# Kernel optimization log

Hardware: AMD Instinct MI355X
Metric: run time of the kernel (lower is better)

Reference implementation:

```python
import jax, jax.numpy as jnp
import numpy as np

NUM_EXPERTS = 64
TOP_K = 2
CAP_FACTOR = 1.0


def setup_inputs() -> dict:
    key = jax.random.key(0)
    k1, k2 = jax.random.split(key)
    x = jax.random.normal(k1, (8192, 4096), dtype=jnp.float32)
    wg = jax.random.normal(k2, (NUM_EXPERTS, 4096), dtype=jnp.float32) * 0.02
    return {"x": x, "wg": wg}


def reference(x, wg):
    # x: [S, M] tokens, wg: [E, M] gate weight (Linear, no bias)
    S, M = x.shape
    E, K = NUM_EXPERTS, TOP_K
    capacity = K * int(CAP_FACTOR * ((S + E - 1) // E))  # static

    logits = jnp.einsum('sm,em->se', x, wg)            # [S, E]
    gates = jax.nn.softmax(logits, axis=1)             # [S, E]
    _, topk_idx = jax.lax.top_k(logits, K)             # [S, K]

    masks = jax.nn.one_hot(topk_idx, E, dtype=x.dtype)  # [S, K, E]
    gates_s = jnp.einsum('se,ske->sk', gates, masks)    # [S, K]

    # load-balancing loss (fp32 path of load_balance)
    me = jnp.sum(gates, axis=0)                         # [E]
    ce = jnp.sum(masks[:, 0], axis=0)                   # [E]
    l_loss = jnp.sum(me * ce) * (E / (S * S))

    # capacity locations: cumsum-sub-one per k, offset by counts of earlier k's
    locs = jnp.cumsum(masks, axis=0) - 1.0              # [S, K, E]
    counts = jnp.sum(masks, axis=0)                     # [K, E]
    acc = jnp.concatenate([jnp.zeros((1, E), x.dtype),
                           jnp.cumsum(counts, axis=0)[:-1]], axis=0)  # [K, E]
    locs = locs + acc[None, :, :]
    loc_s = jnp.einsum('ske,ske->sk', locs, masks).astype(jnp.int32)  # [S, K]

    # postnorm gate normalization (top_k > 1)
    eps = jnp.finfo(gates_s.dtype).eps
    gates_n = gates_s / jnp.clip(jnp.sum(gates_s, axis=1, keepdims=True), eps)

    idx = topk_idx.astype(jnp.int32)                    # [S, K]
    valid = (loc_s >= 0) & (loc_s < capacity)           # [S, K]
    pos = jnp.where(valid, idx * capacity + loc_s, 0)   # [S, K] flat slot ids

    # encode: scatter tokens (unweighted, is_postnorm=True) into [E*capacity, M]
    contrib = jnp.where(valid[..., None], x[:, None, :], 0.0)  # [S, K, M]
    dispatched = jnp.zeros((E * capacity, M), x.dtype)
    dispatched = dispatched.at[pos.reshape(-1)].add(contrib.reshape(-1, M))

    # expert_fn = identity (world_size=1, routing pipeline is the op under test)
    expert_output = dispatched                          # [E*capacity, M]

    # decode: gather back and combine with normalized gates
    gathered = expert_output[pos.reshape(-1)].reshape(S, K, M)
    out = jnp.einsum('sk,skm->sm', gates_n * valid.astype(x.dtype), gathered)
    return out, l_loss
```

## Files before the change

kernel.cpp:

```cpp
#include <hip/hip_runtime.h>
#include <math.h>

#define S_TOK 8192
#define M_DIM 4096
#define NEXP 64
#define CAPACITY 256
#define NCHUNK 128
#define KS 8
#define KSL 512
#define BT 64
#define BK 32
#define NC (KSL / BK)

__global__ __launch_bounds__(256) void k_logits(
    const float* __restrict__ x, const float* __restrict__ wg,
    float* __restrict__ part)
{
    __shared__ float xs[2][BK * 64];
    __shared__ float wsl[2][BK * 64];
    const int tid = threadIdx.x;
    const int tile = blockIdx.x >> 3;
    const int ks   = blockIdx.x & 7;
    const int t0 = tile * BT;
    const int kb = ks * KSL;

    const int tx = tid & 15;
    const int ty = tid >> 4;

    float4 rx[2], rw[2];
    auto ld = [&](int kc) {
        #pragma unroll
        for (int i = 0; i < 2; ++i) {
            const int item = tid + 256 * i;
            const int r = item >> 3, kq = item & 7;
            rx[i] = *(const float4*)(x  + (size_t)(t0 + r) * M_DIM + kc + 4 * kq);
            rw[i] = *(const float4*)(wg + (size_t)r       * M_DIM + kc + 4 * kq);
        }
    };
    auto st = [&](int buf) {
        #pragma unroll
        for (int i = 0; i < 2; ++i) {
            const int item = tid + 256 * i;
            const int r = item >> 3, kq = item & 7;
            const int quad = r >> 2, lo = r & 3;
            const float vx[4] = {rx[i].x, rx[i].y, rx[i].z, rx[i].w};
            const float vw[4] = {rw[i].x, rw[i].y, rw[i].z, rw[i].w};
            #pragma unroll
            for (int j = 0; j < 4; ++j) {
                const int row = 4 * kq + j;
                const int addr = row * 64 + ((quad ^ kq) << 2) + lo;
                xs[buf][addr]  = vx[j];
                wsl[buf][addr] = vw[j];
            }
        }
    };

    float acc[4][4] = {};
    ld(kb);
    st(0);
    __syncthreads();
    for (int c = 0; c < NC; ++c) {
        const int buf = c & 1;
        if (c + 1 < NC) ld(kb + (c + 1) * BK);
        #pragma unroll 8
        for (int kk = 0; kk < BK; ++kk) {
            const int sw = kk >> 2;
            const float4 a = *(const float4*)&xs [buf][kk * 64 + ((ty ^ sw) << 2)];
            const float4 b = *(const float4*)&wsl[buf][kk * 64 + ((tx ^ sw) << 2)];
            const float av[4] = {a.x, a.y, a.z, a.w};
            const float bv[4] = {b.x, b.y, b.z, b.w};
            #pragma unroll
            for (int i = 0; i < 4; ++i)
                #pragma unroll
                for (int j = 0; j < 4; ++j)
                    acc[i][j] = fmaf(av[i], bv[j], acc[i][j]);
        }
        __syncthreads();
        if (c + 1 < NC) st(buf ^ 1);
        __syncthreads();
    }

    #pragma unroll
    for (int i = 0; i < 4; ++i) {
        float4 v;
        v.x = acc[i][0]; v.y = acc[i][1]; v.z = acc[i][2]; v.w = acc[i][3];
        *(float4*)(part + ((size_t)ks * S_TOK + t0 + 4 * ty + i) * NEXP + 4 * tx) = v;
    }
}

__global__ __launch_bounds__(256) void k_reduce(
    const float* __restrict__ part, float* __restrict__ me_g,
    int* __restrict__ idx0_g, int* __restrict__ idx1_g,
    float* __restrict__ gn0_g, float* __restrict__ gn1_g)
{
    __shared__ float me_sh[NEXP];
    const int tid = threadIdx.x;
    if (tid < NEXP) me_sh[tid] = 0.f;
    __syncthreads();

    const int wv = tid >> 6, lane = tid & 63;
    float me_acc = 0.f;
    for (int i = 0; i < 8; ++i) {
        const int t = blockIdx.x * 32 + wv * 8 + i;
        float lg = 0.f;
        #pragma unroll
        for (int s = 0; s < KS; ++s)
            lg += part[((size_t)s * S_TOK + t) * NEXP + lane];

        float v = lg; int id = lane;
        #pragma unroll
        for (int off = 32; off > 0; off >>= 1) {
            float v2 = __shfl_xor(v, off);
            int   i2 = __shfl_xor(id, off);
            if (v2 > v || (v2 == v && i2 < id)) { v = v2; id = i2; }
        }
        const float mx = v; const int i0 = id;

        const float p = expf(lg - mx);
        float sum = p;
        #pragma unroll
        for (int off = 32; off > 0; off >>= 1) sum += __shfl_xor(sum, off);
        me_acc += p / sum;

        float v1 = (lane == i0) ? -INFINITY : lg; int id1 = lane;
        #pragma unroll
        for (int off = 32; off > 0; off >>= 1) {
            float v2 = __shfl_xor(v1, off);
            int   i2 = __shfl_xor(id1, off);
            if (v2 > v1 || (v2 == v1 && i2 < id1)) { v1 = v2; id1 = i2; }
        }

        const float g0 = 1.0f / sum;
        const float g1 = expf(v1 - mx) / sum;
        const float den = fmaxf(g0 + g1, 1.1920929e-07f);
        if (lane == 0) {
            idx0_g[t] = i0;
            idx1_g[t] = id1;
            gn0_g[t] = g0 / den;
            gn1_g[t] = g1 / den;
        }
    }
    atomicAdd(&me_sh[lane], me_acc);
    __syncthreads();
    if (tid < NEXP) atomicAdd(&me_g[tid], me_sh[tid]);
}

__global__ __launch_bounds__(64) void k_rank(
    const int* __restrict__ idx0_g, const int* __restrict__ idx1_g,
    int* __restrict__ rank0_g, int* __restrict__ rank1_g,
    int* __restrict__ cnt_g )
{
    const int lane = threadIdx.x;
    const int chunk = blockIdx.x;
    const int s = chunk * 64 + lane;
    const int e0 = idx0_g[s], e1 = idx1_g[s];
    const unsigned long long lt = (1ull << lane) - 1ull;

    int r0 = 0, r1 = 0, c0 = 0, c1 = 0;
    #pragma unroll
    for (int e = 0; e < 64; ++e) {
        unsigned long long m0 = __ballot(e0 == e);
        unsigned long long m1 = __ballot(e1 == e);
        if (e0 == e) r0 = __popcll(m0 & lt);
        if (e1 == e) r1 = __popcll(m1 & lt);
        if (lane == e) { c0 = __popcll(m0); c1 = __popcll(m1); }
    }
    rank0_g[s] = r0;
    rank1_g[s] = r1;
    cnt_g[chunk * 64 + lane] = c0;
    cnt_g[NCHUNK * 64 + chunk * 64 + lane] = c1;
}

__global__ __launch_bounds__(256) void k_scan(
    const int* __restrict__ cnt_g, int* __restrict__ base_g,
    int* __restrict__ tot0_g, const float* __restrict__ me_g,
    float* __restrict__ loss_out)
{
    const int wv = threadIdx.x >> 6, lane = threadIdx.x & 63;
    const int g = blockIdx.x * 4 + wv;
    const int k = g >> 6, e = g & 63;

    const int c0 = cnt_g[(k * NCHUNK + 2 * lane)     * 64 + e];
    const int c1 = cnt_g[(k * NCHUNK + 2 * lane + 1) * 64 + e];
    const int s = c0 + c1;
    int incl = s;
    #pragma unroll
    for (int d = 1; d < 64; d <<= 1) {
        int v = __shfl_up(incl, d);
        if (lane >= d) incl += v;
    }
    const int excl = incl - s;
    base_g[(k * NCHUNK + 2 * lane)     * 64 + e] = excl;
    base_g[(k * NCHUNK + 2 * lane + 1) * 64 + e] = excl + c0;
    const int total = __shfl(incl, 63);
    if (k == 0 && lane == 0) {
        tot0_g[e] = total;
        atomicAdd(loss_out, me_g[e] * (float)total * 9.5367431640625e-07f);
    }
}

__global__ __launch_bounds__(256) void k_weight(
    const int* __restrict__ idx0_g, const int* __restrict__ idx1_g,
    const float* __restrict__ gn0_g, const float* __restrict__ gn1_g,
    const int* __restrict__ rank0_g, const int* __restrict__ rank1_g,
    const int* __restrict__ base_g, const int* __restrict__ tot0_g,
    float* __restrict__ w_g)
{
    const int s = blockIdx.x * 256 + threadIdx.x;
    const int chunk = s >> 6;
    const int e0 = idx0_g[s], e1 = idx1_g[s];
    const int loc0 = base_g[chunk * 64 + e0] + rank0_g[s];
    const int loc1 = base_g[(NCHUNK + chunk) * 64 + e1] + rank1_g[s] + tot0_g[e1];
    float w = 0.f;
    if (loc0 < CAPACITY) w += gn0_g[s];
    if (loc1 < CAPACITY) w += gn1_g[s];
    w_g[s] = w;
}

__global__ __launch_bounds__(256) void k_out(
    const float* __restrict__ x, const float* __restrict__ w_g,
    float* __restrict__ out)
{
    const int s = blockIdx.x;
    const float w = w_g[s];
    const float4* xr = (const float4*)(x + (size_t)s * M_DIM);
    float4* o = (float4*)(out + (size_t)s * M_DIM);
    #pragma unroll
    for (int i = 0; i < 4; ++i) {
        float4 v = xr[threadIdx.x + 256 * i];
        v.x *= w; v.y *= w; v.z *= w; v.w *= w;
        o[threadIdx.x + 256 * i] = v;
    }
}

extern "C" void kernel_launch(void* const* d_in, const int* in_sizes, int n_in,
                              void* d_out, int out_size, void* d_ws, size_t ws_size,
                              hipStream_t stream)
{
    const float* x  = (const float*)d_in[0];
    const float* wg = (const float*)d_in[1];
    float* out = (float*)d_out;
    float* loss = out + (size_t)S_TOK * M_DIM;

    float* part = (float*)d_ws;
    float* me   = part + (size_t)KS * S_TOK * NEXP;
    int*  idx0  = (int*)(me + NEXP);
    int*  idx1  = idx0 + S_TOK;
    float* gn0  = (float*)(idx1 + S_TOK);
    float* gn1  = gn0 + S_TOK;
    int*  rank0 = (int*)(gn1 + S_TOK);
    int*  rank1 = rank0 + S_TOK;
    int*  cnt   = rank1 + S_TOK;
    int*  base  = cnt + 2 * NCHUNK * 64;
    int*  tot0  = base + 2 * NCHUNK * 64;
    float* wtok = (float*)(tot0 + NEXP);

    hipMemsetAsync(me, 0, NEXP * sizeof(float), stream);
    hipMemsetAsync(loss, 0, sizeof(float), stream);

    k_logits<<<128 * KS, 256, 0, stream>>>(x, wg, part);
    k_reduce<<<S_TOK / 32, 256, 0, stream>>>(part, me, idx0, idx1, gn0, gn1);
    k_rank<<<NCHUNK, 64, 0, stream>>>(idx0, idx1, rank0, rank1, cnt);
    k_scan<<<32, 256, 0, stream>>>(cnt, base, tot0, me, loss);
    k_weight<<<S_TOK / 256, 256, 0, stream>>>(idx0, idx1, gn0, gn1,
                                              rank0, rank1, base, tot0, wtok);
    k_out<<<S_TOK, 256, 0, stream>>>(x, wtok, out);
}
```

Before: 310.8 us.

## Restructure logits GEMM to stream gate weights, fuse routing and scan kernels

The logits kernel now stages only x in LDS (XOR-swizzled per token), and each wave reads 16 expert rows of wg directly from global/cache as float4s, so each thread computes one token against 16 experts. The reduce and rank kernels are merged into a per-chunk routing kernel that packs indices and ranks into one int. The scan, loss and weight kernels are merged into a single 1024-thread block. This cuts launch count and intermediate global traffic. The risks are a serialized single-block finish stage and heavier global loads of wg inside the GEMM inner loop.

```diff
diff --git a/kernel.cpp b/kernel.cpp
--- a/kernel.cpp
+++ b/kernel.cpp
@@ -8,100 +8,105 @@
 #define NCHUNK 128
 #define KS 8
 #define KSL 512
-#define BT 64
-#define BK 32
-#define NC (KSL / BK)
+#define BKL 32
+#define NCL (KSL / BKL)
 
 __global__ __launch_bounds__(256) void k_logits(
     const float* __restrict__ x, const float* __restrict__ wg,
     float* __restrict__ part)
 {
-    __shared__ float xs[2][BK * 64];
-    __shared__ float wsl[2][BK * 64];
+    __shared__ float xt[2][BKL * 64];
     const int tid = threadIdx.x;
     const int tile = blockIdx.x >> 3;
-    const int ks   = blockIdx.x & 7;
-    const int t0 = tile * BT;
+    const int ks = blockIdx.x & 7;
+    const int t0 = tile * 64;
     const int kb = ks * KSL;
-
-    const int tx = tid & 15;
-    const int ty = tid >> 4;
-
-    float4 rx[2], rw[2];
+    const int wave = __builtin_amdgcn_readfirstlane(tid >> 6);
+    const int lane = tid & 63;
+    const int e0 = wave * 16;
+
+    float4 rx[2];
     auto ld = [&](int kc) {
         #pragma unroll
         for (int i = 0; i < 2; ++i) {
             const int item = tid + 256 * i;
-            const int r = item >> 3, kq = item & 7;
-            rx[i] = *(const float4*)(x  + (size_t)(t0 + r) * M_DIM + kc + 4 * kq);
-            rw[i] = *(const float4*)(wg + (size_t)r       * M_DIM + kc + 4 * kq);
+            const int tok = item >> 3, kq = item & 7;
+            rx[i] = *(const float4*)(x + (size_t)(t0 + tok) * M_DIM + kc + 4 * kq);
         }
     };
     auto st = [&](int buf) {
         #pragma unroll
         for (int i = 0; i < 2; ++i) {
             const int item = tid + 256 * i;
-            const int r = item >> 3, kq = item & 7;
-            const int quad = r >> 2, lo = r & 3;
-            const float vx[4] = {rx[i].x, rx[i].y, rx[i].z, rx[i].w};
-            const float vw[4] = {rw[i].x, rw[i].y, rw[i].z, rw[i].w};
+            const int tok = item >> 3, kq = item & 7;
+            const float v[4] = {rx[i].x, rx[i].y, rx[i].z, rx[i].w};
             #pragma unroll
             for (int j = 0; j < 4; ++j) {
-                const int row = 4 * kq + j;
-                const int addr = row * 64 + ((quad ^ kq) << 2) + lo;
-                xs[buf][addr]  = vx[j];
-                wsl[buf][addr] = vw[j];
+                const int k = 4 * kq + j;
+                xt[buf][k * 64 + (tok ^ k)] = v[j];
             }
         }
     };
 
-    float acc[4][4] = {};
+    float acc[16] = {};
     ld(kb);
     st(0);
     __syncthreads();
-    for (int c = 0; c < NC; ++c) {
+    for (int c = 0; c < NCL; ++c) {
         const int buf = c & 1;
-        if (c + 1 < NC) ld(kb + (c + 1) * BK);
-        #pragma unroll 8
-        for (int kk = 0; kk < BK; ++kk) {
-            const int sw = kk >> 2;
-            const float4 a = *(const float4*)&xs [buf][kk * 64 + ((ty ^ sw) << 2)];
-            const float4 b = *(const float4*)&wsl[buf][kk * 64 + ((tx ^ sw) << 2)];
-            const float av[4] = {a.x, a.y, a.z, a.w};
-            const float bv[4] = {b.x, b.y, b.z, b.w};
-            #pragma unroll
-            for (int i = 0; i < 4; ++i)
-                #pragma unroll
-                for (int j = 0; j < 4; ++j)
-                    acc[i][j] = fmaf(av[i], bv[j], acc[i][j]);
+        if (c + 1 < NCL) ld(kb + (c + 1) * BKL);
+        const float* wrow = wg + (size_t)e0 * M_DIM + kb + c * BKL;
+        #pragma unroll
+        for (int k4 = 0; k4 < BKL; k4 += 4) {
+            float4 wv[16];
+            #pragma unroll
+            for (int e = 0; e < 16; ++e)
+                wv[e] = *(const float4*)(wrow + (size_t)e * M_DIM + k4);
+            float a[4];
+            #pragma unroll
+            for (int j = 0; j < 4; ++j) {
+                const int k = k4 + j;
+                a[j] = xt[buf][k * 64 + (lane ^ k)];
+            }
+            #pragma unroll
+            for (int e = 0; e < 16; ++e) {
+                acc[e] = fmaf(a[0], wv[e].x, acc[e]);
+                acc[e] = fmaf(a[1], wv[e].y, acc[e]);
+                acc[e] = fmaf(a[2], wv[e].z, acc[e]);
+                acc[e] = fmaf(a[3], wv[e].w, acc[e]);
+            }
         }
         __syncthreads();
-        if (c + 1 < NC) st(buf ^ 1);
+        if (c + 1 < NCL) st(buf ^ 1);
         __syncthreads();
     }
-
-    #pragma unroll
-    for (int i = 0; i < 4; ++i) {
+    float* po = part + ((size_t)ks * S_TOK + t0 + lane) * NEXP + e0;
+    #pragma unroll
+    for (int j = 0; j < 4; ++j) {
         float4 v;
-        v.x = acc[i][0]; v.y = acc[i][1]; v.z = acc[i][2]; v.w = acc[i][3];
-        *(float4*)(part + ((size_t)ks * S_TOK + t0 + 4 * ty + i) * NEXP + 4 * tx) = v;
-    }
-}
-
-__global__ __launch_bounds__(256) void k_reduce(
+        v.x = acc[4*j]; v.y = acc[4*j+1]; v.z = acc[4*j+2]; v.w = acc[4*j+3];
+        *(float4*)(po + 4 * j) = v;
+    }
+}
+
+__global__ __launch_bounds__(256) void k_route(
     const float* __restrict__ part, float* __restrict__ me_g,
-    int* __restrict__ idx0_g, int* __restrict__ idx1_g,
-    float* __restrict__ gn0_g, float* __restrict__ gn1_g)
+    int* __restrict__ pack_g, float* __restrict__ g0_g, float* __restrict__ g1_g,
+    int* __restrict__ cnt_g )
 {
     __shared__ float me_sh[NEXP];
+    __shared__ int   idxs[64];
+    __shared__ float g0s[64], g1s[64];
     const int tid = threadIdx.x;
+    const int wv = tid >> 6, lane = tid & 63;
+    const int chunk = blockIdx.x;
     if (tid < NEXP) me_sh[tid] = 0.f;
     __syncthreads();
 
-    const int wv = tid >> 6, lane = tid & 63;
     float me_acc = 0.f;
-    for (int i = 0; i < 8; ++i) {
-        const int t = blockIdx.x * 32 + wv * 8 + i;
+    for (int i = 0; i < 16; ++i) {
+        const int tl = wv * 16 + i;
+        const int t = chunk * 64 + tl;
         float lg = 0.f;
         #pragma unroll
         for (int s = 0; s < KS; ++s)
@@ -134,87 +139,96 @@
         const float g1 = expf(v1 - mx) / sum;
         const float den = fmaxf(g0 + g1, 1.1920929e-07f);
         if (lane == 0) {
-            idx0_g[t] = i0;
-            idx1_g[t] = id1;
-            gn0_g[t] = g0 / den;
-            gn1_g[t] = g1 / den;
+            idxs[tl] = i0 | (id1 << 8);
+            g0s[tl] = g0 / den;
+            g1s[tl] = g1 / den;
         }
     }
     atomicAdd(&me_sh[lane], me_acc);
     __syncthreads();
     if (tid < NEXP) atomicAdd(&me_g[tid], me_sh[tid]);
-}
-
-__global__ __launch_bounds__(64) void k_rank(
-    const int* __restrict__ idx0_g, const int* __restrict__ idx1_g,
-    int* __restrict__ rank0_g, int* __restrict__ rank1_g,
-    int* __restrict__ cnt_g )
-{
-    const int lane = threadIdx.x;
-    const int chunk = blockIdx.x;
-    const int s = chunk * 64 + lane;
-    const int e0 = idx0_g[s], e1 = idx1_g[s];
-    const unsigned long long lt = (1ull << lane) - 1ull;
-
-    int r0 = 0, r1 = 0, c0 = 0, c1 = 0;
-    #pragma unroll
-    for (int e = 0; e < 64; ++e) {
-        unsigned long long m0 = __ballot(e0 == e);
-        unsigned long long m1 = __ballot(e1 == e);
-        if (e0 == e) r0 = __popcll(m0 & lt);
-        if (e1 == e) r1 = __popcll(m1 & lt);
-        if (lane == e) { c0 = __popcll(m0); c1 = __popcll(m1); }
-    }
-    rank0_g[s] = r0;
-    rank1_g[s] = r1;
-    cnt_g[chunk * 64 + lane] = c0;
-    cnt_g[NCHUNK * 64 + chunk * 64 + lane] = c1;
-}
-
-__global__ __launch_bounds__(256) void k_scan(
-    const int* __restrict__ cnt_g, int* __restrict__ base_g,
-    int* __restrict__ tot0_g, const float* __restrict__ me_g,
-    float* __restrict__ loss_out)
-{
-    const int wv = threadIdx.x >> 6, lane = threadIdx.x & 63;
-    const int g = blockIdx.x * 4 + wv;
-    const int k = g >> 6, e = g & 63;
-
-    const int c0 = cnt_g[(k * NCHUNK + 2 * lane)     * 64 + e];
-    const int c1 = cnt_g[(k * NCHUNK + 2 * lane + 1) * 64 + e];
-    const int s = c0 + c1;
-    int incl = s;
-    #pragma unroll
-    for (int d = 1; d < 64; d <<= 1) {
-        int v = __shfl_up(incl, d);
-        if (lane >= d) incl += v;
-    }
-    const int excl = incl - s;
-    base_g[(k * NCHUNK + 2 * lane)     * 64 + e] = excl;
-    base_g[(k * NCHUNK + 2 * lane + 1) * 64 + e] = excl + c0;
-    const int total = __shfl(incl, 63);
-    if (k == 0 && lane == 0) {
-        tot0_g[e] = total;
-        atomicAdd(loss_out, me_g[e] * (float)total * 9.5367431640625e-07f);
-    }
-}
-
-__global__ __launch_bounds__(256) void k_weight(
-    const int* __restrict__ idx0_g, const int* __restrict__ idx1_g,
-    const float* __restrict__ gn0_g, const float* __restrict__ gn1_g,
-    const int* __restrict__ rank0_g, const int* __restrict__ rank1_g,
-    const int* __restrict__ base_g, const int* __restrict__ tot0_g,
-    float* __restrict__ w_g)
-{
-    const int s = blockIdx.x * 256 + threadIdx.x;
-    const int chunk = s >> 6;
-    const int e0 = idx0_g[s], e1 = idx1_g[s];
-    const int loc0 = base_g[chunk * 64 + e0] + rank0_g[s];
-    const int loc1 = base_g[(NCHUNK + chunk) * 64 + e1] + rank1_g[s] + tot0_g[e1];
-    float w = 0.f;
-    if (loc0 < CAPACITY) w += gn0_g[s];
-    if (loc1 < CAPACITY) w += gn1_g[s];
-    w_g[s] = w;
+
+    if (wv == 0) {
+        const int pk = idxs[lane];
+        const int e0 = pk & 255, e1 = pk >> 8;
+        const unsigned long long lt = (1ull << lane) - 1ull;
+        int r0 = 0, r1 = 0, c0 = 0, c1 = 0;
+        #pragma unroll
+        for (int e = 0; e < 64; ++e) {
+            unsigned long long m0 = __ballot(e0 == e);
+            unsigned long long m1 = __ballot(e1 == e);
+            if (e0 == e) r0 = __popcll(m0 & lt);
+            if (e1 == e) r1 = __popcll(m1 & lt);
+            if (lane == e) { c0 = __popcll(m0); c1 = __popcll(m1); }
+        }
+        const int s = chunk * 64 + lane;
+        pack_g[s] = e0 | (e1 << 8) | (r0 << 16) | (r1 << 24);
+        g0_g[s] = g0s[lane];
+        g1_g[s] = g1s[lane];
+        cnt_g[chunk * 64 + lane] = c0;
+        cnt_g[(NCHUNK + chunk) * 64 + lane] = c1;
+    }
+}
+
+__global__ __launch_bounds__(1024) void k_finish(
+    const int* __restrict__ cnt_g, const int* __restrict__ pack_g,
+    const float* __restrict__ g0_g, const float* __restrict__ g1_g,
+    const float* __restrict__ me_g, float* __restrict__ wtok,
+    float* __restrict__ loss)
+{
+    __shared__ unsigned short base16[2][NCHUNK][NEXP];
+    __shared__ int ssum[8][128];
+    __shared__ int tot0s[NEXP];
+    __shared__ float lred[NEXP];
+    const int tid = threadIdx.x;
+    const int pair = tid & 127, seg = tid >> 7;
+    const int k = pair >> 6, e = pair & 63;
+
+    int cv[16], s = 0;
+    #pragma unroll
+    for (int c = 0; c < 16; ++c) {
+        cv[c] = cnt_g[(k * NCHUNK + seg * 16 + c) * 64 + e];
+        s += cv[c];
+    }
+    ssum[seg][pair] = s;
+    __syncthreads();
+
+    int segbase = 0, total = 0;
+    #pragma unroll
+    for (int s2 = 0; s2 < 8; ++s2) {
+        const int v = ssum[s2][pair];
+        if (s2 < seg) segbase += v;
+        total += v;
+    }
+    if (k == 0 && seg == 0) tot0s[e] = total;
+    int run = segbase;
+    #pragma unroll
+    for (int c = 0; c < 16; ++c) {
+        base16[k][seg * 16 + c][e] = (unsigned short)run;
+        run += cv[c];
+    }
+    __syncthreads();
+
+    if (tid < NEXP) lred[tid] = me_g[tid] * (float)tot0s[tid];
+    __syncthreads();
+    if (tid == 0) {
+        float t = 0.f;
+        for (int i = 0; i < NEXP; ++i) t += lred[i];
+        *loss = t * 9.5367431640625e-07f;
+    }
+
+    #pragma unroll
+    for (int j = 0; j < 8; ++j) {
+        const int t = j * 1024 + tid;
+        const int pk = pack_g[t];
+        const int e0 = pk & 63, e1 = (pk >> 8) & 63;
+        const int r0 = (pk >> 16) & 255, r1 = (pk >> 24) & 255;
+        const int ch = t >> 6;
+        float w = 0.f;
+        if ((int)base16[0][ch][e0] + r0 < CAPACITY) w += g0_g[t];
+        if ((int)base16[1][ch][e1] + tot0s[e1] + r1 < CAPACITY) w += g1_g[t];
+        wtok[t] = w;
+    }
 }
 
 __global__ __launch_bounds__(256) void k_out(
@@ -244,25 +258,16 @@
 
     float* part = (float*)d_ws;
     float* me   = part + (size_t)KS * S_TOK * NEXP;
-    int*  idx0  = (int*)(me + NEXP);
-    int*  idx1  = idx0 + S_TOK;
-    float* gn0  = (float*)(idx1 + S_TOK);
-    float* gn1  = gn0 + S_TOK;
-    int*  rank0 = (int*)(gn1 + S_TOK);
-    int*  rank1 = rank0 + S_TOK;
-    int*  cnt   = rank1 + S_TOK;
-    int*  base  = cnt + 2 * NCHUNK * 64;
-    int*  tot0  = base + 2 * NCHUNK * 64;
-    float* wtok = (float*)(tot0 + NEXP);
+    int*  pack  = (int*)(me + NEXP);
+    float* g0   = (float*)(pack + S_TOK);
+    float* g1   = g0 + S_TOK;
+    int*  cnt   = (int*)(g1 + S_TOK);
+    float* wtok = (float*)(cnt + 2 * NCHUNK * 64);
 
     hipMemsetAsync(me, 0, NEXP * sizeof(float), stream);
-    hipMemsetAsync(loss, 0, sizeof(float), stream);
 
     k_logits<<<128 * KS, 256, 0, stream>>>(x, wg, part);
-    k_reduce<<<S_TOK / 32, 256, 0, stream>>>(part, me, idx0, idx1, gn0, gn1);
-    k_rank<<<NCHUNK, 64, 0, stream>>>(idx0, idx1, rank0, rank1, cnt);
-    k_scan<<<32, 256, 0, stream>>>(cnt, base, tot0, me, loss);
-    k_weight<<<S_TOK / 256, 256, 0, stream>>>(idx0, idx1, gn0, gn1,
-                                              rank0, rank1, base, tot0, wtok);
+    k_route<<<NCHUNK, 256, 0, stream>>>(part, me, pack, g0, g1, cnt);
+    k_finish<<<1, 1024, 0, stream>>>(cnt, pack, g0, g1, me, wtok, loss);
     k_out<<<S_TOK, 256, 0, stream>>>(x, wtok, out);
 }
```

New measurement: 380.4 us. +22.4%, slower.
